# Kernel tuning notes

Hardware: AMD Instinct MI355X
Metric: run time of the kernel (lower is better)

## Reference

```python
import jax, jax.numpy as jnp
import numpy as np

B, H, S, D = 4, 16, 2048, 64
TEMPERATURE = 8.0  # sqrt(d_k)
NEG_INF = -1e9


def setup_inputs() -> dict:
    key = jax.random.key(0)
    kq, kk, kv, kb = jax.random.split(key, 4)
    q = jax.random.normal(kq, (B, H, S, D), dtype=jnp.float32)
    k = jax.random.normal(kk, (B, H, S, D), dtype=jnp.float32)
    v = jax.random.normal(kv, (B, H, S, D), dtype=jnp.float32)
    mask = jnp.ones((B, 1, S, S), dtype=jnp.int32)
    attn_bias = jax.random.normal(kb, (B, H, S, S), dtype=jnp.float32)
    return {"q": q, "k": k, "v": v, "mask": mask, "attn_bias": attn_bias}


def reference(q, k, v, mask, attn_bias):
    # scores: [B,H,S,S]
    attn = jnp.einsum("bhqd,bhkd->bhqk", q / TEMPERATURE, k)
    attn = jnp.where(mask == 0, NEG_INF, attn)
    attn = attn + attn_bias
    # dropout p=0.0 -> identity
    norm_attn = jax.nn.softmax(attn, axis=-1)
    output = jnp.einsum("bhqk,bhkd->bhqd", norm_attn, v)
    return (output, attn)
```

## Files before the change

### kernel.cpp

```cpp
#include <hip/hip_runtime.h>
#include <math.h>

#define NBATCH 4
#define NHEAD  16
#define SEQ    2048
#define HDIM   64
#define QT     64
#define KT     64
#define NTILE  (SEQ / KT)
#define PSHIFT 8.0f

using f4v = __attribute__((ext_vector_type(4))) float;
using i4v = __attribute__((ext_vector_type(4))) int;
using h4  = __attribute__((ext_vector_type(4))) _Float16;
using h8  = __attribute__((ext_vector_type(8))) _Float16;

__global__ __launch_bounds__(256) void fused_attn_v11(
    const float* __restrict__ qp, const float* __restrict__ kp,
    const float* __restrict__ vp, const int* __restrict__ maskp,
    const float* __restrict__ biasp, float* __restrict__ outp,
    float* __restrict__ attnp)
{
    __shared__ _Float16 s_tile[QT][72];
    __shared__ _Float16 ksh[2][KT][72];
    __shared__ _Float16 vsT[2][HDIM][72];

    const int t    = threadIdx.x;
    const int w    = t >> 6;
    const int lane = t & 63;
    const int g    = lane >> 4;
    const int r    = lane & 15;

    const int bh = blockIdx.y;
    const int b  = bh >> 4;
    const int q0 = blockIdx.x * QT;

    const int r0 = 16 * w + 4 * g;
    const int c0 = r << 2;

    const float* qg    = qp    + ((size_t)bh * SEQ + q0) * HDIM;
    const float* kg    = kp    + (size_t)bh * SEQ * HDIM;
    const float* vg    = vp    + (size_t)bh * SEQ * HDIM;
    const float* biasg = biasp + ((size_t)bh * SEQ + q0) * SEQ;
    const int*   maskg = maskp + ((size_t)b  * SEQ + q0) * SEQ;
    float*       attng = attnp + ((size_t)bh * SEQ + q0) * SEQ;
    float*       outg  = outp  + ((size_t)bh * SEQ + q0) * HDIM;

    h8 qf[2];
    {
        const float* p8 = qg + (16 * w + r) * HDIM;
        #pragma unroll
        for (int s = 0; s < 2; ++s) {
            f4v lo = *reinterpret_cast<const f4v*>(p8 + 32 * s + 8 * g);
            f4v hi = *reinterpret_cast<const f4v*>(p8 + 32 * s + 8 * g + 4);
            #pragma unroll
            for (int j = 0; j < 4; ++j) {
                qf[s][j]     = (_Float16)(0.125f * lo[j]);
                qf[s][j + 4] = (_Float16)(0.125f * hi[j]);
            }
        }
    }

    f4v  oacc[4];
    float l_i[4];
    #pragma unroll
    for (int i = 0; i < 4; ++i) { oacc[i] = (f4v){0.f,0.f,0.f,0.f}; l_i[i] = 0.f; }

    f4v   kreg[4];
    float vreg[16];

    auto issue_loads = [&](int tt) {
        const int k0 = tt * KT;
        #pragma unroll
        for (int it = 0; it < 4; ++it) {
            int i   = t + (it << 8);
            int key = i >> 4;
            int c4  = (i & 15) << 2;
            kreg[it] = *reinterpret_cast<const f4v*>(kg + (size_t)(k0 + key) * HDIM + c4);
        }
        #pragma unroll
        for (int it = 0; it < 4; ++it) {
            int kb = 4 * it + w;
            #pragma unroll
            for (int j = 0; j < 4; ++j)
                vreg[4 * it + j] = vg[(size_t)(k0 + 4 * kb + j) * HDIM + lane];
        }
    };

    auto write_stage = [&](int buf) {
        #pragma unroll
        for (int it = 0; it < 4; ++it) {
            int i   = t + (it << 8);
            int key = i >> 4;
            int c4  = (i & 15) << 2;
            h4 kh = { (_Float16)kreg[it][0], (_Float16)kreg[it][1],
                      (_Float16)kreg[it][2], (_Float16)kreg[it][3] };
            *reinterpret_cast<h4*>(&ksh[buf][key][c4]) = kh;
        }
        #pragma unroll
        for (int it = 0; it < 4; ++it) {
            int kb = 4 * it + w;
            h4 vh = { (_Float16)vreg[4*it+0], (_Float16)vreg[4*it+1],
                      (_Float16)vreg[4*it+2], (_Float16)vreg[4*it+3] };
            *reinterpret_cast<h4*>(&vsT[buf][lane][4 * kb]) = vh;
        }
    };

    auto issue_bm = [&](int tt, f4v* bv, i4v* mv) {
        const int k0 = tt * KT;
        #pragma unroll
        for (int i = 0; i < 4; ++i) {
            size_t rowoff = (size_t)(r0 + i) * SEQ + k0 + c0;
            mv[i] = *reinterpret_cast<const i4v*>(maskg + rowoff);
            bv[i] = *reinterpret_cast<const f4v*>(biasg + rowoff);
        }
    };

    auto compute = [&](int tt, int buf, f4v* bvC, i4v* mvC) {
        const int k0 = tt * KT;
        f4v acc[4];
        #pragma unroll
        for (int tc = 0; tc < 4; ++tc) acc[tc] = (f4v){0.f,0.f,0.f,0.f};
        #pragma unroll
        for (int tc = 0; tc < 4; ++tc) {
            #pragma unroll
            for (int s = 0; s < 2; ++s) {
                h8 kf = *reinterpret_cast<const h8*>(&ksh[buf][16 * tc + r][32 * s + 8 * g]);
                acc[tc] = __builtin_amdgcn_mfma_f32_16x16x32_f16(qf[s], kf, acc[tc], 0, 0, 0);
            }
        }
        #pragma unroll
        for (int tc = 0; tc < 4; ++tc) {
            #pragma unroll
            for (int j = 0; j < 4; ++j)
                s_tile[r0 + j][16 * tc + r] = (_Float16)acc[tc][j];
        }
        #pragma unroll
        for (int i = 0; i < 4; ++i) {
            size_t rowoff = (size_t)(r0 + i) * SEQ + k0 + c0;
            h4 sh = *reinterpret_cast<const h4*>(&s_tile[r0 + i][c0]);
            f4v sc;
            #pragma unroll
            for (int j = 0; j < 4; ++j)
                sc[j] = (mvC[i][j] == 0 ? -1e9f : (float)sh[j]) + bvC[i][j];
            *reinterpret_cast<f4v*>(attng + rowoff) = sc;
            f4v p;
            #pragma unroll
            for (int j = 0; j < 4; ++j) { p[j] = __expf(sc[j] - PSHIFT); l_i[i] += p[j]; }
            h4 ph = { (_Float16)p[0], (_Float16)p[1], (_Float16)p[2], (_Float16)p[3] };
            *reinterpret_cast<h4*>(&s_tile[r0 + i][c0]) = ph;
        }
        #pragma unroll
        for (int s = 0; s < 2; ++s) {
            h8 pf = *reinterpret_cast<const h8*>(&s_tile[16 * w + r][32 * s + 8 * g]);
            #pragma unroll
            for (int tc = 0; tc < 4; ++tc) {
                h8 vf = *reinterpret_cast<const h8*>(&vsT[buf][16 * tc + r][32 * s + 8 * g]);
                oacc[tc] = __builtin_amdgcn_mfma_f32_16x16x32_f16(pf, vf, oacc[tc], 0, 0, 0);
            }
        }
    };

    f4v bA[4], bB[4]; i4v mA[4], mB[4];
    issue_loads(0);
    issue_bm(0, bA, mA);
    write_stage(0);
    __syncthreads();

    for (int t2 = 0; t2 < NTILE; t2 += 2) {
        {
            issue_loads(t2 + 1);
            issue_bm(t2 + 1, bB, mB);
            compute(t2, 0, bA, mA);
            write_stage(1);
            __syncthreads();
        }
        {
            const bool more = (t2 + 2 < NTILE);
            if (more) { issue_loads(t2 + 2); issue_bm(t2 + 2, bA, mA); }
            compute(t2 + 1, 1, bB, mB);
            if (more) write_stage(0);
            __syncthreads();
        }
    }

    #pragma unroll
    for (int i = 0; i < 4; ++i) {
        #pragma unroll
        for (int off = 1; off < 16; off <<= 1)
            l_i[i] += __shfl_xor(l_i[i], off);
    }
    #pragma unroll
    for (int jr = 0; jr < 4; ++jr) {
        float inv = 1.f / l_i[jr];
        #pragma unroll
        for (int tc = 0; tc < 4; ++tc)
            outg[(size_t)(r0 + jr) * HDIM + 16 * tc + r] = oacc[tc][jr] * inv;
    }
}

extern "C" void kernel_launch(void* const* d_in, const int* in_sizes, int n_in,
                              void* d_out, int out_size, void* d_ws, size_t ws_size,
                              hipStream_t stream) {
    const float* q    = (const float*)d_in[0];
    const float* k    = (const float*)d_in[1];
    const float* v    = (const float*)d_in[2];
    const int*   mask = (const int*)  d_in[3];
    const float* bias = (const float*)d_in[4];
    float* out  = (float*)d_out;
    float* attn = out + (size_t)NBATCH * NHEAD * SEQ * HDIM;

    dim3 grid(SEQ / QT, NBATCH * NHEAD);
    fused_attn_v11<<<grid, dim3(256), 0, stream>>>(q, k, v, mask, bias, out, attn);
}
```

Baseline: 565.5 us.

## Process two 64-row query subtiles per block to share K/V tiles

Each block now covers 128 query rows as two 64-row subtiles that reuse the same K/V tiles staged in LDS. This halves K/V global loads and staging work per query row, and halves the grid size. To keep register pressure manageable, the prefetched mask is packed into a bitmask and the prefetched bias is held in fp16. The fp16 bias lowers the precision of the returned attention scores, and the extra per-thread state may reduce occupancy.

```diff
diff --git a/kernel.cpp b/kernel.cpp
--- a/kernel.cpp
+++ b/kernel.cpp
@@ -5,7 +5,7 @@
 #define NHEAD  16
 #define SEQ    2048
 #define HDIM   64
-#define QT     64
+#define QTB    128
 #define KT     64
 #define NTILE  (SEQ / KT)
 #define PSHIFT 8.0f
@@ -15,13 +15,13 @@
 using h4  = __attribute__((ext_vector_type(4))) _Float16;
 using h8  = __attribute__((ext_vector_type(8))) _Float16;
 
-__global__ __launch_bounds__(256) void fused_attn_v11(
+__global__ __launch_bounds__(256) void fused_attn_v13(
     const float* __restrict__ qp, const float* __restrict__ kp,
     const float* __restrict__ vp, const int* __restrict__ maskp,
     const float* __restrict__ biasp, float* __restrict__ outp,
     float* __restrict__ attnp)
 {
-    __shared__ _Float16 s_tile[QT][72];
+    __shared__ _Float16 s_tile[64][72];
     __shared__ _Float16 ksh[2][KT][72];
     __shared__ _Float16 vsT[2][HDIM][72];
 
@@ -33,7 +33,7 @@
 
     const int bh = blockIdx.y;
     const int b  = bh >> 4;
-    const int q0 = blockIdx.x * QT;
+    const int q0 = blockIdx.x * QTB;
 
     const int r0 = 16 * w + 4 * g;
     const int c0 = r << 2;
@@ -46,9 +46,11 @@
     float*       attng = attnp + ((size_t)bh * SEQ + q0) * SEQ;
     float*       outg  = outp  + ((size_t)bh * SEQ + q0) * HDIM;
 
-    h8 qf[2];
-    {
-        const float* p8 = qg + (16 * w + r) * HDIM;
+    h8 qfA[2], qfB[2];
+    #pragma unroll
+    for (int sub = 0; sub < 2; ++sub) {
+        const float* p8 = qg + (64 * sub + 16 * w + r) * HDIM;
+        h8* qf = sub ? qfB : qfA;
         #pragma unroll
         for (int s = 0; s < 2; ++s) {
             f4v lo = *reinterpret_cast<const f4v*>(p8 + 32 * s + 8 * g);
@@ -61,10 +63,13 @@
         }
     }
 
-    f4v  oacc[4];
-    float l_i[4];
-    #pragma unroll
-    for (int i = 0; i < 4; ++i) { oacc[i] = (f4v){0.f,0.f,0.f,0.f}; l_i[i] = 0.f; }
+    f4v  oA[4], oB[4];
+    float lA[4], lB[4];
+    #pragma unroll
+    for (int i = 0; i < 4; ++i) {
+        oA[i] = (f4v){0.f,0.f,0.f,0.f}; oB[i] = (f4v){0.f,0.f,0.f,0.f};
+        lA[i] = 0.f; lB[i] = 0.f;
+    }
 
     f4v   kreg[4];
     float vreg[16];
@@ -106,18 +111,32 @@
         }
     };
 
-    auto issue_bm = [&](int tt, f4v* bv, i4v* mv) {
+    auto issue_bm = [&](int tt, h4* bvA, h4* bvB, unsigned& mAo, unsigned& mBo) {
         const int k0 = tt * KT;
+        unsigned ma = 0, mb = 0;
         #pragma unroll
         for (int i = 0; i < 4; ++i) {
-            size_t rowoff = (size_t)(r0 + i) * SEQ + k0 + c0;
-            mv[i] = *reinterpret_cast<const i4v*>(maskg + rowoff);
-            bv[i] = *reinterpret_cast<const f4v*>(biasg + rowoff);
-        }
-    };
-
-    auto compute = [&](int tt, int buf, f4v* bvC, i4v* mvC) {
-        const int k0 = tt * KT;
+            size_t roA = (size_t)(r0 + i) * SEQ + k0 + c0;
+            i4v mvA = *reinterpret_cast<const i4v*>(maskg + roA);
+            f4v bfA = *reinterpret_cast<const f4v*>(biasg + roA);
+            bvA[i] = (h4){ (_Float16)bfA[0], (_Float16)bfA[1],
+                           (_Float16)bfA[2], (_Float16)bfA[3] };
+            size_t roB = roA + (size_t)64 * SEQ;
+            i4v mvB = *reinterpret_cast<const i4v*>(maskg + roB);
+            f4v bfB = *reinterpret_cast<const f4v*>(biasg + roB);
+            bvB[i] = (h4){ (_Float16)bfB[0], (_Float16)bfB[1],
+                           (_Float16)bfB[2], (_Float16)bfB[3] };
+            #pragma unroll
+            for (int j = 0; j < 4; ++j) {
+                ma |= (mvA[j] != 0 ? 1u : 0u) << (4 * i + j);
+                mb |= (mvB[j] != 0 ? 1u : 0u) << (4 * i + j);
+            }
+        }
+        mAo = ma; mBo = mb;
+    };
+
+    auto compute_sub = [&](int k0, int buf, const h8* qf, const h4* bv,
+                           unsigned mbits, float* l, f4v* oacc, size_t rshift) {
         f4v acc[4];
         #pragma unroll
         for (int tc = 0; tc < 4; ++tc) acc[tc] = (f4v){0.f,0.f,0.f,0.f};
@@ -137,16 +156,17 @@
         }
         #pragma unroll
         for (int i = 0; i < 4; ++i) {
-            size_t rowoff = (size_t)(r0 + i) * SEQ + k0 + c0;
+            size_t rowoff = rshift + (size_t)(r0 + i) * SEQ + k0 + c0;
             h4 sh = *reinterpret_cast<const h4*>(&s_tile[r0 + i][c0]);
             f4v sc;
             #pragma unroll
             for (int j = 0; j < 4; ++j)
-                sc[j] = (mvC[i][j] == 0 ? -1e9f : (float)sh[j]) + bvC[i][j];
+                sc[j] = (((mbits >> (4 * i + j)) & 1) ? (float)sh[j] : -1e9f)
+                        + (float)bv[i][j];
             *reinterpret_cast<f4v*>(attng + rowoff) = sc;
             f4v p;
             #pragma unroll
-            for (int j = 0; j < 4; ++j) { p[j] = __expf(sc[j] - PSHIFT); l_i[i] += p[j]; }
+            for (int j = 0; j < 4; ++j) { p[j] = __expf(sc[j] - PSHIFT); l[i] += p[j]; }
             h4 ph = { (_Float16)p[0], (_Float16)p[1], (_Float16)p[2], (_Float16)p[3] };
             *reinterpret_cast<h4*>(&s_tile[r0 + i][c0]) = ph;
         }
@@ -161,25 +181,28 @@
         }
     };
 
-    f4v bA[4], bB[4]; i4v mA[4], mB[4];
+    h4 bA0[4], bB0[4], bA1[4], bB1[4];
+    unsigned mA0, mB0, mA1, mB1;
     issue_loads(0);
-    issue_bm(0, bA, mA);
+    issue_bm(0, bA0, bB0, mA0, mB0);
     write_stage(0);
     __syncthreads();
 
     for (int t2 = 0; t2 < NTILE; t2 += 2) {
         {
             issue_loads(t2 + 1);
-            issue_bm(t2 + 1, bB, mB);
-            compute(t2, 0, bA, mA);
+            issue_bm(t2 + 1, bA1, bB1, mA1, mB1);
+            compute_sub(t2 * KT, 0, qfA, bA0, mA0, lA, oA, 0);
             write_stage(1);
+            compute_sub(t2 * KT, 0, qfB, bB0, mB0, lB, oB, (size_t)64 * SEQ);
             __syncthreads();
         }
         {
             const bool more = (t2 + 2 < NTILE);
-            if (more) { issue_loads(t2 + 2); issue_bm(t2 + 2, bA, mA); }
-            compute(t2 + 1, 1, bB, mB);
+            if (more) { issue_loads(t2 + 2); issue_bm(t2 + 2, bA0, bB0, mA0, mB0); }
+            compute_sub((t2 + 1) * KT, 1, qfA, bA1, mA1, lA, oA, 0);
             if (more) write_stage(0);
+            compute_sub((t2 + 1) * KT, 1, qfB, bB1, mB1, lB, oB, (size_t)64 * SEQ);
             __syncthreads();
         }
     }
@@ -187,15 +210,20 @@
     #pragma unroll
     for (int i = 0; i < 4; ++i) {
         #pragma unroll
-        for (int off = 1; off < 16; off <<= 1)
-            l_i[i] += __shfl_xor(l_i[i], off);
+        for (int off = 1; off < 16; off <<= 1) {
+            lA[i] += __shfl_xor(lA[i], off);
+            lB[i] += __shfl_xor(lB[i], off);
+        }
     }
     #pragma unroll
     for (int jr = 0; jr < 4; ++jr) {
-        float inv = 1.f / l_i[jr];
-        #pragma unroll
-        for (int tc = 0; tc < 4; ++tc)
-            outg[(size_t)(r0 + jr) * HDIM + 16 * tc + r] = oacc[tc][jr] * inv;
+        float invA = 1.f / lA[jr];
+        float invB = 1.f / lB[jr];
+        #pragma unroll
+        for (int tc = 0; tc < 4; ++tc) {
+            outg[(size_t)(r0 + jr) * HDIM + 16 * tc + r]        = oA[tc][jr] * invA;
+            outg[(size_t)(64 + r0 + jr) * HDIM + 16 * tc + r]   = oB[tc][jr] * invB;
+        }
     }
 }
 
@@ -210,6 +238,6 @@
     float* out  = (float*)d_out;
     float* attn = out + (size_t)NBATCH * NHEAD * SEQ * HDIM;
 
-    dim3 grid(SEQ / QT, NBATCH * NHEAD);
-    fused_attn_v11<<<grid, dim3(256), 0, stream>>>(q, k, v, mask, bias, out, attn);
+    dim3 grid(SEQ / QTB, NBATCH * NHEAD);
+    fused_attn_v13<<<grid, dim3(256), 0, stream>>>(q, k, v, mask, bias, out, attn);
 }
```

Result: slower. 921.7 us (+63.0%).
